# Kernel optimization log

Hardware: AMD Instinct MI355X
Metric: run time of the kernel (lower is better)

The kernel has to match this reference:

```python
import jax, jax.numpy as jnp
import numpy as np

T = 524288          # 2**19 hash table size per level (power of 2)
F = 2               # features per table entry
NL = [16, 22, 30, 42, 58, 80, 111, 153, 212, 293, 406, 561, 775, 1071, 1481, 2046]
L_DIR = 4           # direction positional encoding freqs: 3 + 2*4*3 = 27
AABB = 3.0
PI1, PI2, PI3 = 1, 2654435761, 805459861
N_PTS = 1000000

_BITS = np.array([[(v >> k) & 1 for k in range(3)] for v in range(8)], dtype=bool)  # [8,3] corner offsets


def _linear(key, fan_in, fan_out):
    lim = 1.0 / np.sqrt(fan_in)
    kw, kb = jax.random.split(key)
    W = jax.random.uniform(kw, (fan_in, fan_out), jnp.float32, -lim, lim)
    b = jax.random.uniform(kb, (fan_out,), jnp.float32, -lim, lim)
    return W, b


def setup_inputs() -> dict:
    key = jax.random.key(0)
    ks = jax.random.split(key, 8)
    x = jax.random.normal(ks[0], (N_PTS, 3), jnp.float32)   # world-space sample points
    d = jax.random.normal(ks[1], (N_PTS, 3), jnp.float32)   # view directions
    tables = (jax.random.uniform(ks[2], (len(NL), T, F), jnp.float32) * 2 - 1) * 1e-4
    dW1, db1 = _linear(ks[3], F * len(NL), 64)
    dW2, db2 = _linear(ks[4], 64, 16)
    cW1, cb1 = _linear(ks[5], 27 + 16, 64)
    cW2, cb2 = _linear(ks[6], 64, 64)
    cW3, cb3 = _linear(ks[7], 64, 3)
    return dict(x=x, d=d, tables=tables, dW1=dW1, db1=db1, dW2=dW2, db2=db2,
                cW1=cW1, cb1=cb1, cW2=cW2, cb2=cb2, cW3=cW3, cb3=cb3)


def _hash_encode(xs, tables):
    # xs: [n,3] in [0,1]^3. Multi-resolution hash grid + trilinear interpolation.
    bits = jnp.asarray(_BITS)  # [8,3] bool
    feats = []
    for i, n in enumerate(NL):
        xn = xs * n
        fl = jnp.floor(xn)
        w = xn - fl                                   # [n,3] trilinear weights
        fl_i = fl.astype(jnp.uint32)
        ce_i = jnp.ceil(xn).astype(jnp.uint32)
        corner = jnp.where(bits[None], ce_i[:, None, :], fl_i[:, None, :])   # [n,8,3]
        # spatial hash: xor of coord * prime, mod T; T is 2**19 so uint32
        # wraparound multiply is exact mod T (bit-mask)
        h = ((corner[..., 0] * jnp.uint32(PI1))
             ^ (corner[..., 1] * jnp.uint32(PI2))
             ^ (corner[..., 2] * jnp.uint32(PI3))) & jnp.uint32(T - 1)       # [n,8]
        vals = tables[i][h]                            # [n,8,F] irregular gather
        wc = jnp.prod(jnp.where(bits[None], w[:, None, :], 1.0 - w[:, None, :]), axis=-1)  # [n,8]
        feats.append(jnp.einsum('nv,nvf->nf', wc, vals))
    return jnp.concatenate(feats, axis=1)              # [n, F*len(NL)] = [n,32]


def _pos_enc(d):
    outs = [d]
    for i in range(L_DIR):
        outs.append(jnp.sin((2.0 ** i) * d))
        outs.append(jnp.cos((2.0 ** i) * d))
    return jnp.concatenate(outs, axis=1)               # [n,27]


def reference(x, d, tables, dW1, db1, dW2, db2, cW1, cb1, cW2, cb2, cW3, cb3):
    xs = x / AABB
    mask = (jnp.abs(xs[:, 0]) < 0.5) & (jnp.abs(xs[:, 1]) < 0.5) & (jnp.abs(xs[:, 2]) < 0.5)
    xs = jnp.clip(xs + 0.5, 0.0, 1.0)                  # out-of-box rows get masked below
    feats = _hash_encode(xs, tables)
    h = jnp.maximum(feats @ dW1 + db1, 0.0) @ dW2 + db2            # [n,16] density MLP
    c_in = jnp.concatenate([h, _pos_enc(d)], axis=1)               # [n,43]
    hid = jnp.maximum(c_in @ cW1 + cb1, 0.0)
    hid = jnp.maximum(hid @ cW2 + cb2, 0.0)
    col = jax.nn.sigmoid(hid @ cW3 + cb3)                          # [n,3]
    color = jnp.where(mask[:, None], col, 0.0)
    log_sigma = jnp.where(mask, h[:, 0], -10000.0)
    return color, jnp.exp(log_sigma)
```

## Files before the change

kernel.cpp:

```cpp
#include <hip/hip_runtime.h>
#include <hip/hip_bf16.h>
#include <stdint.h>

#define TS 524288u
#define TMASK (TS - 1u)
#define QTOTAL 331757
#define NHL 11

typedef __attribute__((ext_vector_type(8))) short bf16x8;
typedef __attribute__((ext_vector_type(4))) float f32x4;

__device__ __forceinline__ short f2bf(float f) {
    union { float f; uint32_t u; } v; v.f = f;
    const uint32_t r = (v.u + 0x7fffu + ((v.u >> 16) & 1u)) >> 16;
    return (short)r;
}
__device__ __forceinline__ uint32_t cvtpk(float a, float b) {
    uint32_t r;
    asm("v_cvt_pk_bf16_f32 %0, %1, %2" : "=v"(r) : "v"(a), "v"(b));
    return r;
}
__device__ __forceinline__ short bf1(float a) { return (short)(cvtpk(a, a) & 0xffffu); }
__device__ __forceinline__ float bflo(uint32_t u) { return __uint_as_float(u << 16); }
__device__ __forceinline__ float bfhi(uint32_t u) { return __uint_as_float(u & 0xffff0000u); }
__device__ __forceinline__ uint32_t pack2(float a, float b) {
    return (uint32_t)(uint16_t)f2bf(a) | ((uint32_t)(uint16_t)f2bf(b) << 16);
}

__constant__ float c_NLf[16] = {16.f,22.f,30.f,42.f,58.f,80.f,111.f,153.f,
                                212.f,293.f,406.f,561.f,775.f,1071.f,1481.f,2046.f};
__constant__ int c_NP1[5]  = {17, 23, 31, 43, 59};
__constant__ int c_QOFF[5] = {0, 4913, 17080, 46871, 126378};

__global__ __launch_bounds__(256)
void cvt_tables_h(const float2* __restrict__ src, uint32_t* __restrict__ dst, int npairs)
{
    const int i = blockIdx.x * 256 + threadIdx.x;
    if (i >= npairs) return;
    const float2 v = src[i];
    dst[i] = pack2(v.x, v.y);
}

__global__ __launch_bounds__(256)
void build_quad(const float2* __restrict__ tbf, uint4* __restrict__ quad)
{
    const int i = blockIdx.x * 256 + threadIdx.x;
    if (i >= QTOTAL) return;
    int l, base;
    if      (i <   4913) { l = 0; base = 0;      }
    else if (i <  17080) { l = 1; base = 4913;   }
    else if (i <  46871) { l = 2; base = 17080;  }
    else if (i < 126378) { l = 3; base = 46871;  }
    else                 { l = 4; base = 126378; }
    const int np1 = c_NP1[l];
    int r = i - base;
    const int z = r % np1; r /= np1;
    const int y = r % np1;
    const int x = r / np1;
    const float2* tb = tbf + (size_t)l * TS;
    const uint32_t hx  = (uint32_t)x;
    const uint32_t hy0 = (uint32_t)y       * 2654435761u;
    const uint32_t hy1 = (uint32_t)(y + 1) * 2654435761u;
    const uint32_t hz0 = (uint32_t)z       * 805459861u;
    const uint32_t hz1 = (uint32_t)(z + 1) * 805459861u;
    const float2 a = tb[(hx ^ hy0 ^ hz0) & TMASK];
    const float2 b = tb[(hx ^ hy0 ^ hz1) & TMASK];
    const float2 c = tb[(hx ^ hy1 ^ hz0) & TMASK];
    const float2 d = tb[(hx ^ hy1 ^ hz1) & TMASK];
    uint4 q;
    q.x = pack2(a.x, a.y);
    q.y = pack2(b.x, b.y);
    q.z = pack2(c.x, c.y);
    q.w = pack2(d.x, d.y);
    quad[i] = q;
}

__device__ __forceinline__ uint32_t enc_pt(const int l, const float sx, const float sy,
                                           const float sz,
                                           const uint32_t* __restrict__ tb16h,
                                           const uint4* __restrict__ qtab)
{
    const float nf = c_NLf[l];
    const float xn0 = sx * nf, xn1 = sy * nf, xn2 = sz * nf;
    const float fl0 = floorf(xn0), fl1 = floorf(xn1), fl2 = floorf(xn2);
    const float w0 = xn0 - fl0, w1 = xn1 - fl1, w2 = xn2 - fl2;
    const uint32_t f0 = (uint32_t)fl0, f1 = (uint32_t)fl1, f2 = (uint32_t)fl2;

    float v0x,v0y,v1x,v1y,v2x,v2y,v3x,v3y,v4x,v4y,v5x,v5y,v6x,v6y,v7x,v7y;

    if (l < 5) {
        const int np1 = c_NP1[l];
        const uint4* qt = qtab + c_QOFF[l];
        const int cell = ((int)f0 * np1 + (int)f1) * np1 + (int)f2;
        const uint4 qa = qt[cell];
        const uint4 qb = qt[cell + np1 * np1];
        v0x = bflo(qa.x); v0y = bfhi(qa.x);
        v4x = bflo(qa.y); v4y = bfhi(qa.y);
        v2x = bflo(qa.z); v2y = bfhi(qa.z);
        v6x = bflo(qa.w); v6y = bfhi(qa.w);
        v1x = bflo(qb.x); v1y = bfhi(qb.x);
        v5x = bflo(qb.y); v5y = bfhi(qb.y);
        v3x = bflo(qb.z); v3y = bfhi(qb.z);
        v7x = bflo(qb.w); v7y = bfhi(qb.w);
    } else {
        const uint32_t c0 = (uint32_t)ceilf(xn0);
        const uint32_t c1 = (uint32_t)ceilf(xn1);
        const uint32_t c2 = (uint32_t)ceilf(xn2);
        const uint32_t hyf = f1 * 2654435761u, hyc = c1 * 2654435761u;
        const uint32_t hzf = f2 * 805459861u,  hzc = c2 * 805459861u;
        const uint32_t* tb = tb16h + (size_t)(l - 5) * TS;
        const uint32_t S0 = hyf ^ hzf, S1 = hyc ^ hzf;
        const uint32_t S2 = hyf ^ hzc, S3 = hyc ^ hzc;

        const uint32_t h0 = (f0 ^ S0) & TMASK;
        const uint32_t h1 = (f0 ^ S1) & TMASK;
        const uint32_t h2 = (f0 ^ S2) & TMASK;
        const uint32_t h3 = (f0 ^ S3) & TMASK;
        const uint2 p0 = *reinterpret_cast<const uint2*>(tb + (h0 & ~1u));
        const uint2 p1 = *reinterpret_cast<const uint2*>(tb + (h1 & ~1u));
        const uint2 p2 = *reinterpret_cast<const uint2*>(tb + (h2 & ~1u));
        const uint2 p3 = *reinterpret_cast<const uint2*>(tb + (h3 & ~1u));
        const uint32_t e0 = (h0 & 1u) ? p0.y : p0.x;
        const uint32_t e2 = (h1 & 1u) ? p1.y : p1.x;
        const uint32_t e4 = (h2 & 1u) ? p2.y : p2.x;
        const uint32_t e6 = (h3 & 1u) ? p3.y : p3.x;
        uint32_t e1 = (h0 & 1u) ? p0.x : p0.y;
        uint32_t e3 = (h1 & 1u) ? p1.x : p1.y;
        uint32_t e5 = (h2 & 1u) ? p2.x : p2.y;
        uint32_t e7 = (h3 & 1u) ? p3.x : p3.y;
        if (f0 & 1u) {
            e1 = tb[(c0 ^ S0) & TMASK];
            e3 = tb[(c0 ^ S1) & TMASK];
            e5 = tb[(c0 ^ S2) & TMASK];
            e7 = tb[(c0 ^ S3) & TMASK];
        }
        v0x = bflo(e0); v0y = bfhi(e0); v1x = bflo(e1); v1y = bfhi(e1);
        v2x = bflo(e2); v2y = bfhi(e2); v3x = bflo(e3); v3y = bfhi(e3);
        v4x = bflo(e4); v4y = bfhi(e4); v5x = bflo(e5); v5y = bfhi(e5);
        v6x = bflo(e6); v6y = bfhi(e6); v7x = bflo(e7); v7y = bfhi(e7);
    }

    const float u0 = 1.0f - w0, u1 = 1.0f - w1, u2 = 1.0f - w2;
    float a0, a1;
    a0 = u0*u1*u2 * v0x;              a1 = u0*u1*u2 * v0y;
    a0 = fmaf(w0*u1*u2, v1x, a0);     a1 = fmaf(w0*u1*u2, v1y, a1);
    a0 = fmaf(u0*w1*u2, v2x, a0);     a1 = fmaf(u0*w1*u2, v2y, a1);
    a0 = fmaf(w0*w1*u2, v3x, a0);     a1 = fmaf(w0*w1*u2, v3y, a1);
    a0 = fmaf(u0*u1*w2, v4x, a0);     a1 = fmaf(u0*u1*w2, v4y, a1);
    a0 = fmaf(w0*u1*w2, v5x, a0);     a1 = fmaf(w0*u1*w2, v5y, a1);
    a0 = fmaf(u0*w1*w2, v6x, a0);     a1 = fmaf(u0*w1*w2, v6y, a1);
    a0 = fmaf(w0*w1*w2, v7x, a0);     a1 = fmaf(w0*w1*w2, v7y, a1);

    return cvtpk(a0, a1);
}

__global__ __launch_bounds__(256)
void ngp_encode_lm(const float* __restrict__ xg, const uint32_t* __restrict__ tb16h,
                   const uint4* __restrict__ qtab, uint32_t* __restrict__ feats_lm,
                   const int n, const unsigned tiles, const int lbase)
{
    const unsigned b = blockIdx.x;
    const int l = lbase + (int)(b / tiles);
    const int p = (int)(b - (unsigned)(l - lbase) * tiles) * 256 + threadIdx.x;
    if (p >= n) return;

    float sx = xg[3*p+0] / 3.0f, sy = xg[3*p+1] / 3.0f, sz = xg[3*p+2] / 3.0f;
    if (!((fabsf(sx) < 0.5f) && (fabsf(sy) < 0.5f) && (fabsf(sz) < 0.5f))) {
        feats_lm[(size_t)l * n + p] = 0u;
        return;
    }
    sx = fminf(fmaxf(sx + 0.5f, 0.0f), 1.0f);
    sy = fminf(fmaxf(sy + 0.5f, 0.0f), 1.0f);
    sz = fminf(fmaxf(sz + 0.5f, 0.0f), 1.0f);
    feats_lm[(size_t)l * n + p] = enc_pt(l, sx, sy, sz, tb16h, qtab);
}

__global__ __launch_bounds__(256)
void ngp_encode_f32(const float* __restrict__ xg, const float2* __restrict__ tbf,
                    uint32_t* __restrict__ feats_lm, const int n, const unsigned tiles)
{
    const unsigned b = blockIdx.x;
    const int l = (int)(b / tiles);
    const int p = (int)(b - (unsigned)l * tiles) * 256 + threadIdx.x;
    if (p >= n) return;
    float sx = xg[3*p+0] / 3.0f, sy = xg[3*p+1] / 3.0f, sz = xg[3*p+2] / 3.0f;
    if (!((fabsf(sx) < 0.5f) && (fabsf(sy) < 0.5f) && (fabsf(sz) < 0.5f))) {
        feats_lm[(size_t)l * n + p] = 0u;
        return;
    }
    sx = fminf(fmaxf(sx + 0.5f, 0.0f), 1.0f);
    sy = fminf(fmaxf(sy + 0.5f, 0.0f), 1.0f);
    sz = fminf(fmaxf(sz + 0.5f, 0.0f), 1.0f);
    const float nf = c_NLf[l];
    const float xn0 = sx*nf, xn1 = sy*nf, xn2 = sz*nf;
    const float fl0 = floorf(xn0), fl1 = floorf(xn1), fl2 = floorf(xn2);
    const float w0 = xn0-fl0, w1 = xn1-fl1, w2 = xn2-fl2;
    const uint32_t f0=(uint32_t)fl0, f1=(uint32_t)fl1, f2=(uint32_t)fl2;
    const uint32_t c0=(uint32_t)ceilf(xn0), c1=(uint32_t)ceilf(xn1), c2=(uint32_t)ceilf(xn2);
    const uint32_t hyf = f1*2654435761u, hyc = c1*2654435761u;
    const uint32_t hzf = f2*805459861u,  hzc = c2*805459861u;
    const float2* tb = tbf + (size_t)l * TS;
    const float2 e0 = tb[(f0^hyf^hzf)&TMASK], e1 = tb[(c0^hyf^hzf)&TMASK];
    const float2 e2 = tb[(f0^hyc^hzf)&TMASK], e3 = tb[(c0^hyc^hzf)&TMASK];
    const float2 e4 = tb[(f0^hyf^hzc)&TMASK], e5 = tb[(c0^hyf^hzc)&TMASK];
    const float2 e6 = tb[(f0^hyc^hzc)&TMASK], e7 = tb[(c0^hyc^hzc)&TMASK];
    const float u0 = 1.0f-w0, u1 = 1.0f-w1, u2 = 1.0f-w2;
    float a0, a1;
    a0 = u0*u1*u2 * e0.x;             a1 = u0*u1*u2 * e0.y;
    a0 = fmaf(w0*u1*u2, e1.x, a0);    a1 = fmaf(w0*u1*u2, e1.y, a1);
    a0 = fmaf(u0*w1*u2, e2.x, a0);    a1 = fmaf(u0*w1*u2, e2.y, a1);
    a0 = fmaf(w0*w1*u2, e3.x, a0);    a1 = fmaf(w0*w1*u2, e3.y, a1);
    a0 = fmaf(u0*u1*w2, e4.x, a0);    a1 = fmaf(u0*u1*w2, e4.y, a1);
    a0 = fmaf(w0*u1*w2, e5.x, a0);    a1 = fmaf(w0*u1*w2, e5.y, a1);
    a0 = fmaf(u0*w1*w2, e6.x, a0);    a1 = fmaf(u0*w1*w2, e6.y, a1);
    a0 = fmaf(w0*w1*w2, e7.x, a0);    a1 = fmaf(w0*w1*w2, e7.y, a1);
    feats_lm[(size_t)l * n + p] = pack2(a0, a1);
}

#define ACT_STRIDE 72

__global__ __launch_bounds__(256, 2)
void ngp_mlp_mfma(const float* __restrict__ xg, const float* __restrict__ dg,
                  const uint32_t* __restrict__ feats_lm,
                  const float* __restrict__ dW1, const float* __restrict__ db1,
                  const float* __restrict__ dW2, const float* __restrict__ db2,
                  const float* __restrict__ cW1, const float* __restrict__ cb1,
                  const float* __restrict__ cW2, const float* __restrict__ cb2,
                  const float* __restrict__ cW3, const float* __restrict__ cb3,
                  float* __restrict__ out, int n)
{
    __shared__ __align__(16) short w1[2048];
    __shared__ __align__(16) short w2[1024];
    __shared__ __align__(16) short w3[4096];
    __shared__ __align__(16) short w4[4096];
    __shared__ __align__(16) short w5[1024];
    __shared__ __align__(16) float b1[64];
    __shared__ __align__(16) float b2[16];
    __shared__ __align__(16) float b3[64];
    __shared__ __align__(16) float b4[64];
    __shared__ __align__(16) float b5[16];
    __shared__ __align__(16) short act[4][16*ACT_STRIDE];

    const int tid = threadIdx.x;

    for (int i2 = tid; i2 < 4*16*ACT_STRIDE/2; i2 += 256)
        reinterpret_cast<uint32_t*>(act)[i2] = 0u;

    for (int i2 = tid; i2 < 2048; i2 += 256) {
        const int jb = i2 >> 9, lane = (i2 >> 3) & 63, e = i2 & 7;
        const int j = jb*16 + (lane & 15), k = ((lane >> 4) << 3) + e;
        w1[i2] = f2bf(dW1[k*64 + j]);
    }
    for (int i2 = tid; i2 < 1024; i2 += 256) {
        const int kb = i2 >> 9, lane = (i2 >> 3) & 63, e = i2 & 7;
        const int j = lane & 15, k = kb*32 + ((lane >> 4) << 3) + e;
        w2[i2] = f2bf(dW2[k*16 + j]);
    }
    for (int i2 = tid; i2 < 4096; i2 += 256) {
        const int jb = i2 >> 10, kb = (i2 >> 9) & 1, lane = (i2 >> 3) & 63, e = i2 & 7;
        const int j = jb*16 + (lane & 15), k = kb*32 + ((lane >> 4) << 3) + e;
        w3[i2] = (k < 43) ? f2bf(cW1[k*64 + j]) : (short)0;
        w4[i2] = f2bf(cW2[k*64 + j]);
    }
    for (int i2 = tid; i2 < 1024; i2 += 256) {
        const int kb = i2 >> 9, lane = (i2 >> 3) & 63, e = i2 & 7;
        const int j = lane & 15, k = kb*32 + ((lane >> 4) << 3) + e;
        w5[i2] = (j < 3) ? f2bf(cW3[k*3 + j]) : (short)0;
    }
    if (tid < 64) { b1[tid] = db1[tid]; b3[tid] = cb1[tid]; b4[tid] = cb2[tid]; }
    if (tid < 16) { b2[tid] = db2[tid]; b5[tid] = (tid < 3) ? cb3[tid] : 0.0f; }
    __syncthreads();

    const int wv = tid >> 6, lane = tid & 63;
    const int p16 = lane & 15, quad = lane >> 4;
    const int dc = (quad < 3) ? quad : 0;
    short* buf = &act[wv][0];

    bf16x8 A1[4], A2[2], A3[8], A4[8], A5[2];
    #pragma unroll
    for (int jb = 0; jb < 4; ++jb) A1[jb] = *reinterpret_cast<const bf16x8*>(&w1[(jb*64 + lane)*8]);
    #pragma unroll
    for (int kb = 0; kb < 2; ++kb) A2[kb] = *reinterpret_cast<const bf16x8*>(&w2[(kb*64 + lane)*8]);
    #pragma unroll
    for (int i = 0; i < 8; ++i) {
        A3[i] = *reinterpret_cast<const bf16x8*>(&w3[(i*64 + lane)*8]);
        A4[i] = *reinterpret_cast<const bf16x8*>(&w4[(i*64 + lane)*8]);
    }
    #pragma unroll
    for (int kb = 0; kb < 2; ++kb) A5[kb] = *reinterpret_cast<const bf16x8*>(&w5[(kb*64 + lane)*8]);

    const int ntiles = (n + 63) >> 6;
    int t = blockIdx.x;
    if (t >= ntiles) return;

    int pp_n; bool valid_n;
    uint32_t fn0, fn1, fn2, fn3;
    float in0, in1, in2, dn;

    auto issue = [&](int tt) {
        const int pr = tt*64 + wv*16 + p16;
        valid_n = (pr < n);
        pp_n = valid_n ? pr : (n - 1);
        fn0 = feats_lm[(size_t)(4*quad+0)*n + pp_n];
        fn1 = feats_lm[(size_t)(4*quad+1)*n + pp_n];
        fn2 = feats_lm[(size_t)(4*quad+2)*n + pp_n];
        fn3 = feats_lm[(size_t)(4*quad+3)*n + pp_n];
        in0 = xg[3*pp_n+0];
        in1 = xg[3*pp_n+1];
        in2 = xg[3*pp_n+2];
        dn  = dg[3*pp_n + dc];
    };

    issue(t);
    while (t < ntiles) {
        const int pp = pp_n;
        const bool valid = valid_n;
        const uint32_t fc0 = fn0, fc1 = fn1, fc2 = fn2, fc3 = fn3;
        const float ic0 = in0, ic1 = in1, ic2 = in2;
        const float dv = dn;

        const int t2 = t + gridDim.x;
        if (t2 < ntiles) issue(t2);

        const bool inside = (fabsf(ic0 / 3.0f) < 0.5f) && (fabsf(ic1 / 3.0f) < 0.5f)
                         && (fabsf(ic2 / 3.0f) < 0.5f);

        union { int4 i; bf16x8 v; } bu;
        bu.i.x = (int)fc0; bu.i.y = (int)fc1; bu.i.z = (int)fc2; bu.i.w = (int)fc3;
        const bf16x8 bA = bu.v;
        #pragma unroll
        for (int jb = 0; jb < 4; ++jb) {
            const int j0 = jb*16 + quad*4;
            f32x4 acc = *reinterpret_cast<const f32x4*>(&b1[j0]);
            acc = __builtin_amdgcn_mfma_f32_16x16x32_bf16(A1[jb], bA, acc, 0, 0, 0);
            uint2 s;
            s.x = cvtpk(fmaxf(acc[0], 0.f), fmaxf(acc[1], 0.f));
            s.y = cvtpk(fmaxf(acc[2], 0.f), fmaxf(acc[3], 0.f));
            *reinterpret_cast<uint2*>(&buf[p16*ACT_STRIDE + j0]) = s;
        }

        {
            const bf16x8 bF0 = *reinterpret_cast<const bf16x8*>(&buf[p16*ACT_STRIDE + quad*8]);
            const bf16x8 bF1 = *reinterpret_cast<const bf16x8*>(&buf[p16*ACT_STRIDE + 32 + quad*8]);
            f32x4 acc2 = *reinterpret_cast<const f32x4*>(&b2[quad*4]);
            acc2 = __builtin_amdgcn_mfma_f32_16x16x32_bf16(A2[0], bF0, acc2, 0, 0, 0);
            acc2 = __builtin_amdgcn_mfma_f32_16x16x32_bf16(A2[1], bF1, acc2, 0, 0, 0);
            if (quad == 0 && valid)
                out[(size_t)3*n + pp] = inside ? __expf(acc2[0]) : 0.0f;
            uint2 s;
            s.x = cvtpk(acc2[0], acc2[1]);
            s.y = cvtpk(acc2[2], acc2[3]);
            *reinterpret_cast<uint2*>(&buf[p16*ACT_STRIDE + quad*4]) = s;
        }
        if (quad < 3) {
            buf[p16*ACT_STRIDE + 16 + quad] = bf1(dv);
            float arg = dv;
            #pragma unroll
            for (int f = 0; f < 4; ++f) {
                buf[p16*ACT_STRIDE + 19 + 6*f + quad] = bf1(__sinf(arg));
                buf[p16*ACT_STRIDE + 22 + 6*f + quad] = bf1(__cosf(arg));
                arg += arg;
            }
        }

        {
            const bf16x8 bF0 = *reinterpret_cast<const bf16x8*>(&buf[p16*ACT_STRIDE + quad*8]);
            const bf16x8 bF1 = *reinterpret_cast<const bf16x8*>(&buf[p16*ACT_STRIDE + 32 + quad*8]);
            #pragma unroll
            for (int jb = 0; jb < 4; ++jb) {
                const int j0 = jb*16 + quad*4;
                f32x4 acc = *reinterpret_cast<const f32x4*>(&b3[j0]);
                acc = __builtin_amdgcn_mfma_f32_16x16x32_bf16(A3[jb*2 + 0], bF0, acc, 0, 0, 0);
                acc = __builtin_amdgcn_mfma_f32_16x16x32_bf16(A3[jb*2 + 1], bF1, acc, 0, 0, 0);
                uint2 s;
                s.x = cvtpk(fmaxf(acc[0], 0.f), fmaxf(acc[1], 0.f));
                s.y = cvtpk(fmaxf(acc[2], 0.f), fmaxf(acc[3], 0.f));
                *reinterpret_cast<uint2*>(&buf[p16*ACT_STRIDE + j0]) = s;
            }
        }

        {
            const bf16x8 bF0 = *reinterpret_cast<const bf16x8*>(&buf[p16*ACT_STRIDE + quad*8]);
            const bf16x8 bF1 = *reinterpret_cast<const bf16x8*>(&buf[p16*ACT_STRIDE + 32 + quad*8]);
            #pragma unroll
            for (int jb = 0; jb < 4; ++jb) {
                const int j0 = jb*16 + quad*4;
                f32x4 acc = *reinterpret_cast<const f32x4*>(&b4[j0]);
                acc = __builtin_amdgcn_mfma_f32_16x16x32_bf16(A4[jb*2 + 0], bF0, acc, 0, 0, 0);
                acc = __builtin_amdgcn_mfma_f32_16x16x32_bf16(A4[jb*2 + 1], bF1, acc, 0, 0, 0);
                uint2 s;
                s.x = cvtpk(fmaxf(acc[0], 0.f), fmaxf(acc[1], 0.f));
                s.y = cvtpk(fmaxf(acc[2], 0.f), fmaxf(acc[3], 0.f));
                *reinterpret_cast<uint2*>(&buf[p16*ACT_STRIDE + j0]) = s;
            }
        }

        {
            const bf16x8 bF0 = *reinterpret_cast<const bf16x8*>(&buf[p16*ACT_STRIDE + quad*8]);
            const bf16x8 bF1 = *reinterpret_cast<const bf16x8*>(&buf[p16*ACT_STRIDE + 32 + quad*8]);
            f32x4 acc5 = *reinterpret_cast<const f32x4*>(&b5[quad*4]);
            acc5 = __builtin_amdgcn_mfma_f32_16x16x32_bf16(A5[0], bF0, acc5, 0, 0, 0);
            acc5 = __builtin_amdgcn_mfma_f32_16x16x32_bf16(A5[1], bF1, acc5, 0, 0, 0);
            if (quad == 0 && valid) {
                #pragma unroll
                for (int r = 0; r < 3; ++r) {
                    const float s = 1.0f / (1.0f + __expf(-acc5[r]));
                    out[3*(size_t)pp + r] = inside ? s : 0.0f;
                }
            }
        }
        t = t2;
    }
}

extern "C" void kernel_launch(void* const* d_in, const int* in_sizes, int n_in,
                              void* d_out, int out_size, void* d_ws, size_t ws_size,
                              hipStream_t stream)
{
    const float* x   = (const float*)d_in[0];
    const float* d   = (const float*)d_in[1];
    const float* tb  = (const float*)d_in[2];
    const float* dW1 = (const float*)d_in[3];
    const float* db1 = (const float*)d_in[4];
    const float* dW2 = (const float*)d_in[5];
    const float* db2 = (const float*)d_in[6];
    const float* cW1 = (const float*)d_in[7];
    const float* cb1 = (const float*)d_in[8];
    const float* cW2 = (const float*)d_in[9];
    const float* cb2 = (const float*)d_in[10];
    const float* cW3 = (const float*)d_in[11];
    const float* cb3 = (const float*)d_in[12];
    float* out = (float*)d_out;

    const int n = in_sizes[0] / 3;

    size_t off = 0;
    uint32_t* feats_lm = (uint32_t*)d_ws;                 off += (size_t)n * 16 * 4;
    uint32_t* tb16h    = (uint32_t*)((char*)d_ws + off);  off += (size_t)NHL * TS * 4;
    uint4*    quadbuf  = (uint4*)((char*)d_ws + off);     off += (size_t)QTOTAL * 16;
    const bool planA = (ws_size >= off);

    const unsigned tiles = (unsigned)((n + 255) / 256);
    const int ntiles = (n + 63) >> 6;
    const int nblk = (ntiles < 512) ? ntiles : 512;

    if (planA) {
        {
            const int npairs = NHL * (int)TS;
            hipLaunchKernelGGL(cvt_tables_h, dim3((npairs + 255) / 256), dim3(256), 0, stream,
                               (const float2*)tb + 5 * (size_t)TS, tb16h, npairs);
        }
        hipLaunchKernelGGL(build_quad, dim3((QTOTAL + 255) / 256), dim3(256), 0, stream,
                           (const float2*)tb, quadbuf);
        hipLaunchKernelGGL(ngp_encode_lm, dim3(tiles * 8), dim3(256), 0, stream,
                           x, tb16h, quadbuf, feats_lm, n, tiles, 0);
        hipLaunchKernelGGL(ngp_encode_lm, dim3(tiles * 8), dim3(256), 0, stream,
                           x, tb16h, quadbuf, feats_lm, n, tiles, 8);
    } else {
        hipLaunchKernelGGL(ngp_encode_f32, dim3(tiles * 16), dim3(256), 0, stream,
                           x, (const float2*)tb, feats_lm, n, tiles);
    }
    hipLaunchKernelGGL(ngp_mlp_mfma, dim3(nblk), dim3(256), 0, stream,
                       x, d, feats_lm, dW1, db1, dW2, db2,
                       cW1, cb1, cW2, cb2, cW3, cb3, out, n);
}
```

Before: 418.3 us.

## Extend dense quad table to level 5 and rework hashed corner gathers

```diff
diff --git a/kernel.cpp b/kernel.cpp
--- a/kernel.cpp
+++ b/kernel.cpp
@@ -4,7 +4,7 @@
 
 #define TS 524288u
 #define TMASK (TS - 1u)
-#define QTOTAL 331757
+#define QTOTAL 863198
 #define NHL 11
 
 typedef __attribute__((ext_vector_type(8))) short bf16x8;
@@ -29,8 +29,8 @@
 
 __constant__ float c_NLf[16] = {16.f,22.f,30.f,42.f,58.f,80.f,111.f,153.f,
                                 212.f,293.f,406.f,561.f,775.f,1071.f,1481.f,2046.f};
-__constant__ int c_NP1[5]  = {17, 23, 31, 43, 59};
-__constant__ int c_QOFF[5] = {0, 4913, 17080, 46871, 126378};
+__constant__ int c_NP1[6]  = {17, 23, 31, 43, 59, 81};
+__constant__ int c_QOFF[6] = {0, 4913, 17080, 46871, 126378, 331757};
 
 __global__ __launch_bounds__(256)
 void cvt_tables_h(const float2* __restrict__ src, uint32_t* __restrict__ dst, int npairs)
@@ -51,7 +51,8 @@
     else if (i <  17080) { l = 1; base = 4913;   }
     else if (i <  46871) { l = 2; base = 17080;  }
     else if (i < 126378) { l = 3; base = 46871;  }
-    else                 { l = 4; base = 126378; }
+    else if (i < 331757) { l = 4; base = 126378; }
+    else                 { l = 5; base = 331757; }
     const int np1 = c_NP1[l];
     int r = i - base;
     const int z = r % np1; r /= np1;
@@ -88,7 +89,7 @@
 
     float v0x,v0y,v1x,v1y,v2x,v2y,v3x,v3y,v4x,v4y,v5x,v5y,v6x,v6y,v7x,v7y;
 
-    if (l < 5) {
+    if (l < 6) {
         const int np1 = c_NP1[l];
         const uint4* qt = qtab + c_QOFF[l];
         const int cell = ((int)f0 * np1 + (int)f1) * np1 + (int)f2;
@@ -109,30 +110,27 @@
         const uint32_t hyf = f1 * 2654435761u, hyc = c1 * 2654435761u;
         const uint32_t hzf = f2 * 805459861u,  hzc = c2 * 805459861u;
         const uint32_t* tb = tb16h + (size_t)(l - 5) * TS;
-        const uint32_t S0 = hyf ^ hzf, S1 = hyc ^ hzf;
-        const uint32_t S2 = hyf ^ hzc, S3 = hyc ^ hzc;
-
-        const uint32_t h0 = (f0 ^ S0) & TMASK;
-        const uint32_t h1 = (f0 ^ S1) & TMASK;
-        const uint32_t h2 = (f0 ^ S2) & TMASK;
-        const uint32_t h3 = (f0 ^ S3) & TMASK;
-        const uint2 p0 = *reinterpret_cast<const uint2*>(tb + (h0 & ~1u));
-        const uint2 p1 = *reinterpret_cast<const uint2*>(tb + (h1 & ~1u));
-        const uint2 p2 = *reinterpret_cast<const uint2*>(tb + (h2 & ~1u));
-        const uint2 p3 = *reinterpret_cast<const uint2*>(tb + (h3 & ~1u));
-        const uint32_t e0 = (h0 & 1u) ? p0.y : p0.x;
-        const uint32_t e2 = (h1 & 1u) ? p1.y : p1.x;
-        const uint32_t e4 = (h2 & 1u) ? p2.y : p2.x;
-        const uint32_t e6 = (h3 & 1u) ? p3.y : p3.x;
-        uint32_t e1 = (h0 & 1u) ? p0.x : p0.y;
-        uint32_t e3 = (h1 & 1u) ? p1.x : p1.y;
-        uint32_t e5 = (h2 & 1u) ? p2.x : p2.y;
-        uint32_t e7 = (h3 & 1u) ? p3.x : p3.y;
-        if (f0 & 1u) {
-            e1 = tb[(c0 ^ S0) & TMASK];
-            e3 = tb[(c0 ^ S1) & TMASK];
-            e5 = tb[(c0 ^ S2) & TMASK];
-            e7 = tb[(c0 ^ S3) & TMASK];
+        const uint32_t Sff = hyf ^ hzf, Scf = hyc ^ hzf;
+        const uint32_t Sfc = hyf ^ hzc, Scc = hyc ^ hzc;
+        uint32_t e0,e1,e2,e3,e4,e5,e6,e7;
+        if ((f0 ^ c0) == 1u) {
+            const uint32_t h0 = (f0 ^ Sff) & TMASK;
+            const uint32_t h2 = (f0 ^ Scf) & TMASK;
+            const uint32_t h4 = (f0 ^ Sfc) & TMASK;
+            const uint32_t h6 = (f0 ^ Scc) & TMASK;
+            const uint2 t0 = *reinterpret_cast<const uint2*>(tb + (h0 & ~1u));
+            const uint2 t2 = *reinterpret_cast<const uint2*>(tb + (h2 & ~1u));
+            const uint2 t4 = *reinterpret_cast<const uint2*>(tb + (h4 & ~1u));
+            const uint2 t6 = *reinterpret_cast<const uint2*>(tb + (h6 & ~1u));
+            e0 = (h0 & 1u) ? t0.y : t0.x;  e1 = (h0 & 1u) ? t0.x : t0.y;
+            e2 = (h2 & 1u) ? t2.y : t2.x;  e3 = (h2 & 1u) ? t2.x : t2.y;
+            e4 = (h4 & 1u) ? t4.y : t4.x;  e5 = (h4 & 1u) ? t4.x : t4.y;
+            e6 = (h6 & 1u) ? t6.y : t6.x;  e7 = (h6 & 1u) ? t6.x : t6.y;
+        } else {
+            e0 = tb[(f0 ^ Sff) & TMASK];  e1 = tb[(c0 ^ Sff) & TMASK];
+            e2 = tb[(f0 ^ Scf) & TMASK];  e3 = tb[(c0 ^ Scf) & TMASK];
+            e4 = tb[(f0 ^ Sfc) & TMASK];  e5 = tb[(c0 ^ Sfc) & TMASK];
+            e6 = tb[(f0 ^ Scc) & TMASK];  e7 = tb[(c0 ^ Scc) & TMASK];
         }
         v0x = bflo(e0); v0y = bfhi(e0); v1x = bflo(e1); v1y = bfhi(e1);
         v2x = bflo(e2); v2y = bfhi(e2); v3x = bflo(e3); v3y = bfhi(e3);
@@ -160,8 +158,9 @@
                    const int n, const unsigned tiles, const int lbase)
 {
     const unsigned b = blockIdx.x;
-    const int l = lbase + (int)(b / tiles);
-    const int p = (int)(b - (unsigned)(l - lbase) * tiles) * 256 + threadIdx.x;
+    const int dl = (int)(b / tiles);
+    const int l = lbase + dl;
+    const int p = (int)(b - (unsigned)dl * tiles) * 256 + threadIdx.x;
     if (p >= n) return;
 
     float sx = xg[3*p+0] / 3.0f, sy = xg[3*p+1] / 3.0f, sz = xg[3*p+2] / 3.0f;
@@ -454,8 +453,10 @@
                            (const float2*)tb, quadbuf);
         hipLaunchKernelGGL(ngp_encode_lm, dim3(tiles * 8), dim3(256), 0, stream,
                            x, tb16h, quadbuf, feats_lm, n, tiles, 0);
-        hipLaunchKernelGGL(ngp_encode_lm, dim3(tiles * 8), dim3(256), 0, stream,
+        hipLaunchKernelGGL(ngp_encode_lm, dim3(tiles * 4), dim3(256), 0, stream,
                            x, tb16h, quadbuf, feats_lm, n, tiles, 8);
+        hipLaunchKernelGGL(ngp_encode_lm, dim3(tiles * 4), dim3(256), 0, stream,
+                           x, tb16h, quadbuf, feats_lm, n, tiles, 12);
     } else {
         hipLaunchKernelGGL(ngp_encode_f32, dim3(tiles * 16), dim3(256), 0, stream,
                            x, (const float2*)tb, feats_lm, n, tiles);
```

New measurement: 387.3 us. 1.08x faster.
